# Optimization experiments

Measured on AMD Instinct MI355X. Metric: run time of the kernel, lower is better.

Reference implementation:

```python
import jax, jax.numpy as jnp
import numpy as np

# ---- Build Cayley tables for projective GA G(3,0,1), basis ordered by grade ----
_BLADES = [(), (0,), (1,), (2,), (3,), (0,1), (0,2), (0,3), (1,2), (1,3), (2,3),
           (0,1,2), (0,1,3), (0,2,3), (1,2,3), (0,1,2,3)]
_IDX = {b: i for i, b in enumerate(_BLADES)}

def _blade_mul(a, b, metric):
    """Multiply basis blades a*b. Returns (sign, result_blade); sign=0 if it vanishes."""
    arr = list(a) + list(b)
    sign = 1
    changed = True
    while changed:
        changed = False
        for i in range(len(arr) - 1):
            if arr[i] > arr[i + 1]:
                arr[i], arr[i + 1] = arr[i + 1], arr[i]
                sign = -sign
                changed = True
            elif arr[i] == arr[i + 1]:
                sign *= metric[arr[i]]
                del arr[i:i + 2]
                changed = True
                break
    return sign, tuple(arr)

def _build_tables():
    metric = [0, 1, 1, 1]  # e0^2 = 0 (degenerate), e1^2=e2^2=e3^2=1
    G = np.zeros((16, 16, 16), np.float32)  # geometric product
    W = np.zeros((16, 16, 16), np.float32)  # outer (wedge) product
    for a in _BLADES:
        for b in _BLADES:
            s, r = _blade_mul(a, b, metric)
            if s != 0:
                G[_IDX[a], _IDX[b], _IDX[r]] = s
            if not (set(a) & set(b)):
                s2, r2 = _blade_mul(a, b, [1, 1, 1, 1])
                W[_IDX[a], _IDX[b], _IDX[r2]] = s2
    # Right-complement dual: dual(e_a) = s * e_c with e_a ^ dual(e_a) = e0123
    full = (0, 1, 2, 3)
    dual_idx = np.zeros(16, np.int32)
    dual_sign = np.zeros(16, np.float32)
    for a in _BLADES:
        c = tuple(sorted(set(full) - set(a)))
        s, _ = _blade_mul(a, c, [1, 1, 1, 1])
        dual_idx[_IDX[a]] = _IDX[c]
        dual_sign[_IDX[a]] = s
    # Coefficient map: dual(x)[j] = dual_sign[dual_idx[j]] * x[dual_idx[j]]
    out_sign = dual_sign[dual_idx]
    return jnp.asarray(G), jnp.asarray(W), jnp.asarray(dual_idx), jnp.asarray(out_sign)

_G, _W, _DUAL_IDX, _DUAL_SIGN = _build_tables()
_PSS = 15  # index of pseudoscalar e0123

def _dual(x):
    return x[..., _DUAL_IDX] * _DUAL_SIGN


def setup_inputs() -> dict:
    key = jax.random.key(0)
    k1, k2, k3 = jax.random.split(key, 3)
    B, T, C = 64, 8192, 16
    return {
        "x": jax.random.normal(k1, (B, T, C), dtype=jnp.float32),
        "y": jax.random.normal(k2, (B, T, C), dtype=jnp.float32),
        "ref": jax.random.normal(k3, (B, T, C), dtype=jnp.float32),
    }


def reference(x, y, ref):
    # Geometric product over the Cayley table
    gp = jnp.einsum("bti,btj,ijk->btk", x, y, _G)
    # E(3)-equivariant join: ref_e0123 * dual(dual(x) ^ dual(y))
    wedge = jnp.einsum("bti,btj,ijk->btk", _dual(x), _dual(y), _W)
    join = ref[..., _PSS:_PSS + 1] * _dual(wedge)
    return jnp.concatenate([gp, join], axis=-1)  # (B, T, 32)
```

## Files before the change

### kernel.cpp

```cpp
#include <hip/hip_runtime.h>

namespace ga {

constexpr int MASK[16]        = {0,1,2,4,8,3,5,9,6,10,12,7,11,13,14,15};
constexpr int IDX_OF_MASK[16] = {0,1,2,5,3,6,8,11,4,7,9,12,10,13,14,15};

constexpr int popc(int v) { int c = 0; while (v) { c += v & 1; v >>= 1; } return c; }

constexpr int reorder_sign(int a, int b) {
    int s = 0; int t = a >> 1;
    while (t) { s += popc(t & b); t >>= 1; }
    return (s & 1) ? -1 : 1;
}

struct Term { signed char i, j, k, s; };

struct GPTab { Term t[192]; };
constexpr GPTab build_gp() {
    GPTab T{}; int n = 0;
    for (int i = 0; i < 16; i++)
        for (int j = 0; j < 16; j++) {
            int a = MASK[i], b = MASK[j];
            if (a & b & 1) continue;
            T.t[n].i = (signed char)i;
            T.t[n].j = (signed char)j;
            T.t[n].k = (signed char)IDX_OF_MASK[a ^ b];
            T.t[n].s = (signed char)reorder_sign(a, b);
            n++;
        }
    return T;
}

struct JNTab { Term t[81]; };
constexpr JNTab build_join() {
    JNTab T{}; int n = 0;
    int didx[16] = {}, dsgn[16] = {};
    for (int i = 0; i < 16; i++) {
        int a = MASK[i], c = (~a) & 0xF;
        didx[i] = IDX_OF_MASK[c];
        dsgn[i] = reorder_sign(a, c);
    }
    for (int i = 0; i < 16; i++)
        for (int j = 0; j < 16; j++) {
            int p = didx[i], q = didx[j];
            int a = MASK[p], b = MASK[q];
            if (a & b) continue;
            int m = IDX_OF_MASK[a | b];
            int k = didx[m];
            int s = dsgn[i] * dsgn[j] * dsgn[m] * reorder_sign(a, b);
            T.t[n].i = (signed char)i;
            T.t[n].j = (signed char)j;
            T.t[n].k = (signed char)k;
            T.t[n].s = (signed char)s;
            n++;
        }
    return T;
}

constexpr GPTab G = build_gp();
constexpr JNTab J = build_join();

}

constexpr int XSTRIDE = 20;
constexpr int OSTRIDE = 36;
constexpr int WAVE_FLOATS = 64 * XSTRIDE * 2 + 64;

__global__ __launch_bounds__(128)
void MVGeometricBilinear_kernel(const float* __restrict__ x,
                                const float* __restrict__ y,
                                const float* __restrict__ ref,
                                float* __restrict__ out,
                                int nwaves)
{
    __shared__ __align__(16) float lds[2 * WAVE_FLOATS];

    const int wave = threadIdx.x >> 6;
    const int lane = threadIdx.x & 63;
    const long wid = (long)blockIdx.x * 2 + wave;
    const bool active = (wid < nwaves);

    float* wl = lds + wave * WAVE_FLOATS;
    float* lx = wl;
    float* ly = wl + 64 * XSTRIDE;
    float* lr = wl + 128 * XSTRIDE;
    float* lo = wl;

    const long wbase = (active ? wid : 0) * 64;

    float xx[16], yy[16], r = 0.f;
    float gp[16] = {0.f, 0.f, 0.f, 0.f, 0.f, 0.f, 0.f, 0.f,
                    0.f, 0.f, 0.f, 0.f, 0.f, 0.f, 0.f, 0.f};
    float jn[16] = {0.f, 0.f, 0.f, 0.f, 0.f, 0.f, 0.f, 0.f,
                    0.f, 0.f, 0.f, 0.f, 0.f, 0.f, 0.f, 0.f};

    if (active) {
        const float4* gx = reinterpret_cast<const float4*>(x)   + wbase * 4;
        const float4* gy = reinterpret_cast<const float4*>(y)   + wbase * 4;
        const float4* gr = reinterpret_cast<const float4*>(ref) + wbase * 4;
#pragma unroll
        for (int c = 0; c < 4; c++) {
            const int g  = lane + 64 * c;
            const int p  = g >> 2;
            const int ch = g & 3;
            const float4 vx = gx[g];
            const float4 vy = gy[g];
            const float4 vr = gr[g];
            *reinterpret_cast<float4*>(lx + p * XSTRIDE + ch * 4) = vx;
            *reinterpret_cast<float4*>(ly + p * XSTRIDE + ch * 4) = vy;
            if (ch == 3) lr[p] = vr.w;
        }

#pragma unroll
        for (int k = 0; k < 4; k++) {
            const float4 vx = *reinterpret_cast<const float4*>(lx + lane * XSTRIDE + k * 4);
            const float4 vy = *reinterpret_cast<const float4*>(ly + lane * XSTRIDE + k * 4);
            xx[4*k+0] = vx.x; xx[4*k+1] = vx.y; xx[4*k+2] = vx.z; xx[4*k+3] = vx.w;
            yy[4*k+0] = vy.x; yy[4*k+1] = vy.y; yy[4*k+2] = vy.z; yy[4*k+3] = vy.w;
        }
        r = lr[lane];

#pragma unroll
        for (int t = 0; t < 192; t++) {
            const int ti = ga::G.t[t].i, tj = ga::G.t[t].j, tk = ga::G.t[t].k;
            const float v = xx[ti] * yy[tj];
            if (ga::G.t[t].s > 0) gp[tk] += v; else gp[tk] -= v;
        }
#pragma unroll
        for (int t = 0; t < 81; t++) {
            const int ti = ga::J.t[t].i, tj = ga::J.t[t].j, tk = ga::J.t[t].k;
            const float v = xx[ti] * yy[tj];
            if (ga::J.t[t].s > 0) jn[tk] += v; else jn[tk] -= v;
        }
    }

    __syncthreads();

    if (active) {
#pragma unroll
        for (int k = 0; k < 4; k++)
            *reinterpret_cast<float4*>(lo + lane * OSTRIDE + k * 4) =
                make_float4(gp[4*k+0], gp[4*k+1], gp[4*k+2], gp[4*k+3]);
#pragma unroll
        for (int k = 0; k < 4; k++)
            *reinterpret_cast<float4*>(lo + lane * OSTRIDE + 16 + k * 4) =
                make_float4(r * jn[4*k+0], r * jn[4*k+1], r * jn[4*k+2], r * jn[4*k+3]);

        float4* go = reinterpret_cast<float4*>(out) + wbase * 8;
#pragma unroll
        for (int c = 0; c < 8; c++) {
            const int g  = lane + 64 * c;
            const int p  = g >> 3;
            const int ch = g & 7;
            go[g] = *reinterpret_cast<const float4*>(lo + p * OSTRIDE + ch * 4);
        }
    }
}

__global__ __launch_bounds__(64)
void MVGeometricBilinear_tail(const float* __restrict__ x,
                              const float* __restrict__ y,
                              const float* __restrict__ ref,
                              float* __restrict__ out,
                              int start, int npts)
{
    int pt = start + blockIdx.x * 64 + threadIdx.x;
    if (pt >= npts) return;
    float xx[16], yy[16];
#pragma unroll
    for (int k = 0; k < 16; k++) { xx[k] = x[(size_t)pt*16+k]; yy[k] = y[(size_t)pt*16+k]; }
    const float r = ref[(size_t)pt*16+15];
    float gp[16] = {}, jn[16] = {};
#pragma unroll
    for (int t = 0; t < 192; t++) {
        const float v = xx[ga::G.t[t].i] * yy[ga::G.t[t].j];
        if (ga::G.t[t].s > 0) gp[ga::G.t[t].k] += v; else gp[ga::G.t[t].k] -= v;
    }
#pragma unroll
    for (int t = 0; t < 81; t++) {
        const float v = xx[ga::J.t[t].i] * yy[ga::J.t[t].j];
        if (ga::J.t[t].s > 0) jn[ga::J.t[t].k] += v; else jn[ga::J.t[t].k] -= v;
    }
#pragma unroll
    for (int k = 0; k < 16; k++) out[(size_t)pt*32+k] = gp[k];
#pragma unroll
    for (int k = 0; k < 16; k++) out[(size_t)pt*32+16+k] = r * jn[k];
}

extern "C" void kernel_launch(void* const* d_in, const int* in_sizes, int n_in,
                              void* d_out, int out_size, void* d_ws, size_t ws_size,
                              hipStream_t stream) {
    const float* x   = (const float*)d_in[0];
    const float* y   = (const float*)d_in[1];
    const float* ref = (const float*)d_in[2];
    float* out = (float*)d_out;

    const int npts   = in_sizes[0] / 16;
    const int nwaves = npts / 64;
    const int blocks = (nwaves + 1) / 2;

    MVGeometricBilinear_kernel<<<blocks, 128, 0, stream>>>(x, y, ref, out, nwaves);

    const int rem = npts - nwaves * 64;
    if (rem > 0) {
        MVGeometricBilinear_tail<<<(rem + 63) / 64, 64, 0, stream>>>(
            x, y, ref, out, nwaves * 64, npts);
    }
}
```

Measured before the change: 149.3 us.

## Make each single-wave block loop over four chunks with register prefetch

Launches one-wave blocks that each process four consecutive 64-point chunks. The next chunk's x/y data and the ref scalar are loaded into registers while the current chunk is computed, so memory latency overlaps with the arithmetic. The ref read now fetches only the needed scalar instead of a full float4 row. LDS is reused across iterations, with compiler barriers in place of __syncthreads, which relies on the block being a single wavefront. The cost is higher register pressure from the prefetch buffers and fewer blocks in flight.

```diff
diff --git a/kernel.cpp b/kernel.cpp
--- a/kernel.cpp
+++ b/kernel.cpp
@@ -64,53 +64,57 @@
 
 constexpr int XSTRIDE = 20;
 constexpr int OSTRIDE = 36;
-constexpr int WAVE_FLOATS = 64 * XSTRIDE * 2 + 64;
-
-__global__ __launch_bounds__(128)
+
+__global__ __launch_bounds__(64)
 void MVGeometricBilinear_kernel(const float* __restrict__ x,
                                 const float* __restrict__ y,
                                 const float* __restrict__ ref,
                                 float* __restrict__ out,
-                                int nwaves)
+                                int nchunks, int niter)
 {
-    __shared__ __align__(16) float lds[2 * WAVE_FLOATS];
-
-    const int wave = threadIdx.x >> 6;
-    const int lane = threadIdx.x & 63;
-    const long wid = (long)blockIdx.x * 2 + wave;
-    const bool active = (wid < nwaves);
-
-    float* wl = lds + wave * WAVE_FLOATS;
-    float* lx = wl;
-    float* ly = wl + 64 * XSTRIDE;
-    float* lr = wl + 128 * XSTRIDE;
-    float* lo = wl;
-
-    const long wbase = (active ? wid : 0) * 64;
-
-    float xx[16], yy[16], r = 0.f;
-    float gp[16] = {0.f, 0.f, 0.f, 0.f, 0.f, 0.f, 0.f, 0.f,
-                    0.f, 0.f, 0.f, 0.f, 0.f, 0.f, 0.f, 0.f};
-    float jn[16] = {0.f, 0.f, 0.f, 0.f, 0.f, 0.f, 0.f, 0.f,
-                    0.f, 0.f, 0.f, 0.f, 0.f, 0.f, 0.f, 0.f};
-
-    if (active) {
-        const float4* gx = reinterpret_cast<const float4*>(x)   + wbase * 4;
-        const float4* gy = reinterpret_cast<const float4*>(y)   + wbase * 4;
-        const float4* gr = reinterpret_cast<const float4*>(ref) + wbase * 4;
+    __shared__ __align__(16) float lds[64 * XSTRIDE * 2];
+
+    const int lane = threadIdx.x;
+    long chunk = (long)blockIdx.x * niter;
+    long cend  = chunk + niter;
+    if (cend > nchunks) cend = nchunks;
+    if (chunk >= cend) return;
+
+    float* lx = lds;
+    float* ly = lds + 64 * XSTRIDE;
+    float* lo = lds;
+
+    float4 cx[4], cy[4]; float cr;
+    {
+        const float4* gx = reinterpret_cast<const float4*>(x) + chunk * 256;
+        const float4* gy = reinterpret_cast<const float4*>(y) + chunk * 256;
+#pragma unroll
+        for (int c = 0; c < 4; c++) { cx[c] = gx[lane + 64*c]; cy[c] = gy[lane + 64*c]; }
+        cr = ref[(chunk * 64 + lane) * 16 + 15];
+    }
+
+    while (true) {
 #pragma unroll
         for (int c = 0; c < 4; c++) {
-            const int g  = lane + 64 * c;
-            const int p  = g >> 2;
-            const int ch = g & 3;
-            const float4 vx = gx[g];
-            const float4 vy = gy[g];
-            const float4 vr = gr[g];
-            *reinterpret_cast<float4*>(lx + p * XSTRIDE + ch * 4) = vx;
-            *reinterpret_cast<float4*>(ly + p * XSTRIDE + ch * 4) = vy;
-            if (ch == 3) lr[p] = vr.w;
-        }
-
+            const int p  = 16*c + (lane >> 2);
+            const int ch = lane & 3;
+            *reinterpret_cast<float4*>(lx + p * XSTRIDE + ch * 4) = cx[c];
+            *reinterpret_cast<float4*>(ly + p * XSTRIDE + ch * 4) = cy[c];
+        }
+        const float r = cr;
+
+        const long next = chunk + 1;
+        const bool pf = (next < cend);
+        float4 nx[4], ny[4]; float nr = 0.f;
+        if (pf) {
+            const float4* gx = reinterpret_cast<const float4*>(x) + next * 256;
+            const float4* gy = reinterpret_cast<const float4*>(y) + next * 256;
+#pragma unroll
+            for (int c = 0; c < 4; c++) { nx[c] = gx[lane + 64*c]; ny[c] = gy[lane + 64*c]; }
+            nr = ref[(next * 64 + lane) * 16 + 15];
+        }
+
+        float xx[16], yy[16];
 #pragma unroll
         for (int k = 0; k < 4; k++) {
             const float4 vx = *reinterpret_cast<const float4*>(lx + lane * XSTRIDE + k * 4);
@@ -118,8 +122,11 @@
             xx[4*k+0] = vx.x; xx[4*k+1] = vx.y; xx[4*k+2] = vx.z; xx[4*k+3] = vx.w;
             yy[4*k+0] = vy.x; yy[4*k+1] = vy.y; yy[4*k+2] = vy.z; yy[4*k+3] = vy.w;
         }
-        r = lr[lane];
-
+
+        float gp[16] = {0.f, 0.f, 0.f, 0.f, 0.f, 0.f, 0.f, 0.f,
+                        0.f, 0.f, 0.f, 0.f, 0.f, 0.f, 0.f, 0.f};
+        float jn[16] = {0.f, 0.f, 0.f, 0.f, 0.f, 0.f, 0.f, 0.f,
+                        0.f, 0.f, 0.f, 0.f, 0.f, 0.f, 0.f, 0.f};
 #pragma unroll
         for (int t = 0; t < 192; t++) {
             const int ti = ga::G.t[t].i, tj = ga::G.t[t].j, tk = ga::G.t[t].k;
@@ -132,11 +139,9 @@
             const float v = xx[ti] * yy[tj];
             if (ga::J.t[t].s > 0) jn[tk] += v; else jn[tk] -= v;
         }
-    }
-
-    __syncthreads();
-
-    if (active) {
+
+        asm volatile("" ::: "memory");
+
 #pragma unroll
         for (int k = 0; k < 4; k++)
             *reinterpret_cast<float4*>(lo + lane * OSTRIDE + k * 4) =
@@ -146,7 +151,7 @@
             *reinterpret_cast<float4*>(lo + lane * OSTRIDE + 16 + k * 4) =
                 make_float4(r * jn[4*k+0], r * jn[4*k+1], r * jn[4*k+2], r * jn[4*k+3]);
 
-        float4* go = reinterpret_cast<float4*>(out) + wbase * 8;
+        float4* go = reinterpret_cast<float4*>(out) + chunk * 512;
 #pragma unroll
         for (int c = 0; c < 8; c++) {
             const int g  = lane + 64 * c;
@@ -154,6 +159,14 @@
             const int ch = g & 7;
             go[g] = *reinterpret_cast<const float4*>(lo + p * OSTRIDE + ch * 4);
         }
+
+        asm volatile("" ::: "memory");
+
+        if (!pf) break;
+#pragma unroll
+        for (int c = 0; c < 4; c++) { cx[c] = nx[c]; cy[c] = ny[c]; }
+        cr = nr;
+        chunk = next;
     }
 }
 
@@ -195,15 +208,19 @@
     const float* ref = (const float*)d_in[2];
     float* out = (float*)d_out;
 
-    const int npts   = in_sizes[0] / 16;
-    const int nwaves = npts / 64;
-    const int blocks = (nwaves + 1) / 2;
-
-    MVGeometricBilinear_kernel<<<blocks, 128, 0, stream>>>(x, y, ref, out, nwaves);
-
-    const int rem = npts - nwaves * 64;
+    const int npts    = in_sizes[0] / 16;
+    const int nchunks = npts / 64;
+    const int niter   = 4;
+    const int blocks  = (nchunks + niter - 1) / niter;
+
+    if (nchunks > 0) {
+        MVGeometricBilinear_kernel<<<blocks, 64, 0, stream>>>(
+            x, y, ref, out, nchunks, niter);
+    }
+
+    const int rem = npts - nchunks * 64;
     if (rem > 0) {
         MVGeometricBilinear_tail<<<(rem + 63) / 64, 64, 0, stream>>>(
-            x, y, ref, out, nwaves * 64, npts);
-    }
-}
+            x, y, ref, out, nchunks * 64, npts);
+    }
+}
```

Measured after the change: 172.5 us. 15.5% more time.
